# Kernel optimization log

Hardware: AMD Instinct MI355X
Metric: run time of the kernel (lower is better)

Reference implementation:

```python
import jax, jax.numpy as jnp
import numpy as np

B = 4_194_304  # batch
M = 4          # num_modes
N = 4          # num_nodes (hardcoded in BistableModeBank)
MU_MIN, MU_MAX = 0.1, 1.5


def setup_inputs() -> dict:
    key = jax.random.key(0)
    k1, k2, k3, k4, k5, k6 = jax.random.split(key, 6)
    return {
        "X": jax.random.normal(k1, (B, N), dtype=jnp.float32),
        "z": jax.random.randint(k2, (B,), 0, M, dtype=jnp.int32),
        "dt_val": jnp.full((1,), 0.01, dtype=jnp.float32),
        # learned params (torch inits them to zeros; small noise for non-degenerate test)
        "graph_logits": 0.1 * jax.random.normal(k3, (M, N, N), dtype=jnp.float32),
        "mu_logits": 0.1 * jax.random.normal(k4, (M, N), dtype=jnp.float32),
        "alpha_param": 0.1 * jax.random.normal(k5, (M,), dtype=jnp.float32),
        "beta_param": 0.1 * jax.random.normal(k6, (M,), dtype=jnp.float32),
    }


def reference(X, z, dt_val, graph_logits, mu_logits, alpha_param, beta_param):
    # graphs(): symmetrize logits, sigmoid, zero diagonal
    S = 0.5 * (graph_logits + jnp.swapaxes(graph_logits, 1, 2))
    W = jax.nn.sigmoid(S) * (1.0 - jnp.eye(N, dtype=X.dtype))  # (M,N,N)
    mus = MU_MIN + (MU_MAX - MU_MIN) * jax.nn.sigmoid(mu_logits)  # (M,N)
    deg = W.sum(axis=-1)  # (M,N)

    # per-item mode routing (replaces boolean-mask gather/scatter of forward_grouped)
    mu_z = mus[z]                        # (B,N)
    deg_z = deg[z]                       # (B,N)
    a_z = alpha_param[z][:, None]        # (B,1)
    b_z = beta_param[z][:, None]         # (B,1)

    local = mu_z * X - X ** 3            # bistable_batch
    # adjacency matmul for all modes, then select routed mode per item
    coup_all = jnp.einsum('mij,bj->bmi', W, X)                       # (B,M,N)
    coup_z = jnp.take_along_axis(coup_all, z[:, None, None], axis=1)[:, 0, :]  # (B,N)

    coupling = a_z * deg_z * X + b_z * coup_z
    dt = dt_val[0]
    return X + dt * (local + coupling)
```

## Files before the change

### kernel.cpp

```cpp
#include <hip/hip_runtime.h>


typedef float fvec4 __attribute__((ext_vector_type(4)));

__global__ __launch_bounds__(256) void bistable_kernel(
    const float* __restrict__ X,
    const int*   __restrict__ z,
    const float* __restrict__ dt_val,
    const float* __restrict__ G,
    const float* __restrict__ mu_logits,
    const float* __restrict__ alpha_p,
    const float* __restrict__ beta_p,
    float* __restrict__ out,
    int Bn)
{
    __shared__ float A[4 * 16];
    __shared__ float s_dt;

    const int t = threadIdx.x;
    if (t < 16) {
        const int m = t >> 2;
        const int i = t & 3;
        const float dt = dt_val[0];
        float w[4];
        float deg = 0.0f;
        #pragma unroll
        for (int j = 0; j < 4; ++j) {
            float s = 0.5f * (G[m * 16 + i * 4 + j] + G[m * 16 + j * 4 + i]);
            float wv = 1.0f / (1.0f + __expf(-s));
            if (j == i) wv = 0.0f;
            w[j] = wv;
            deg += wv;
        }
        const float mu = 0.1f + 1.4f / (1.0f + __expf(-mu_logits[m * 4 + i]));
        const float a = alpha_p[m];
        const float b = beta_p[m];
        float arow[4];
        #pragma unroll
        for (int j = 0; j < 4; ++j) arow[j] = dt * b * w[j];
        arow[i] = 1.0f + dt * (mu + a * deg);
        #pragma unroll
        for (int j = 0; j < 4; ++j) A[m * 16 + i * 4 + j] = arow[j];
    }
    if (t == 0) s_dt = dt_val[0];
    __syncthreads();

    const float dt = s_dt;
    const fvec4* __restrict__ X4 = (const fvec4*)X;
    fvec4* __restrict__ O4 = (fvec4*)out;

    const int tid = blockIdx.x * blockDim.x + t;
    const int stride = gridDim.x * blockDim.x;

    auto body = [&](const fvec4& xv, int m, fvec4& ov) {
        const float* __restrict__ a = &A[m * 16];
        const float x0 = xv.x, x1 = xv.y, x2 = xv.z, x3 = xv.w;
        ov.x = a[0]  * x0 + a[1]  * x1 + a[2]  * x2 + a[3]  * x3 - dt * x0 * x0 * x0;
        ov.y = a[4]  * x0 + a[5]  * x1 + a[6]  * x2 + a[7]  * x3 - dt * x1 * x1 * x1;
        ov.z = a[8]  * x0 + a[9]  * x1 + a[10] * x2 + a[11] * x3 - dt * x2 * x2 * x2;
        ov.w = a[12] * x0 + a[13] * x1 + a[14] * x2 + a[15] * x3 - dt * x3 * x3 * x3;
    };

    int idx = tid;
    for (; idx + 3 * stride < Bn; idx += 4 * stride) {
        const int i0 = idx, i1 = idx + stride, i2 = idx + 2 * stride, i3 = idx + 3 * stride;
        const fvec4 x0 = X4[i0];
        const fvec4 x1 = X4[i1];
        const fvec4 x2 = X4[i2];
        const fvec4 x3 = X4[i3];
        const int m0 = z[i0], m1 = z[i1], m2 = z[i2], m3 = z[i3];
        fvec4 o0, o1, o2, o3;
        body(x0, m0, o0);
        body(x1, m1, o1);
        body(x2, m2, o2);
        body(x3, m3, o3);
        __builtin_nontemporal_store(o0, &O4[i0]);
        __builtin_nontemporal_store(o1, &O4[i1]);
        __builtin_nontemporal_store(o2, &O4[i2]);
        __builtin_nontemporal_store(o3, &O4[i3]);
    }
    for (; idx < Bn; idx += stride) {
        const fvec4 xv = X4[idx];
        const int m = z[idx];
        fvec4 ov;
        body(xv, m, ov);
        __builtin_nontemporal_store(ov, &O4[idx]);
    }
}

extern "C" void kernel_launch(void* const* d_in, const int* in_sizes, int n_in,
                              void* d_out, int out_size, void* d_ws, size_t ws_size,
                              hipStream_t stream) {
    const float* X         = (const float*)d_in[0];
    const int*   z         = (const int*)d_in[1];
    const float* dt_val    = (const float*)d_in[2];
    const float* G         = (const float*)d_in[3];
    const float* mu_logits = (const float*)d_in[4];
    const float* alpha_p   = (const float*)d_in[5];
    const float* beta_p    = (const float*)d_in[6];
    float* out = (float*)d_out;

    const int Bn = in_sizes[1];

    const int block = 256;
    int grid = (Bn + block - 1) / block;
    if (grid > 4096) grid = 4096;

    bistable_kernel<<<grid, block, 0, stream>>>(X, z, dt_val, G, mu_logits,
                                                alpha_p, beta_p, out, Bn);
}
```

Before: 29.36 us.

## Software-pipeline grid-stride loop with two-deep register prefetch and halve grid cap

Replaces the 4-way unrolled grid-stride loop with a software-pipelined loop. Each thread keeps the current item and the next one in registers and issues the load for the item two strides ahead before computing and storing the current one. The grid cap drops from 4096 to 2048 blocks, so each thread handles more iterations. The aim is to keep loads in flight continuously, but there are fewer independent loads per thread than with the 4-way unroll, and the smaller grid may reduce memory-level parallelism on a bandwidth-bound kernel.

Measured after the change: 28.24 us. -3.8%, faster.

```diff
diff --git a/kernel.cpp b/kernel.cpp
--- a/kernel.cpp
+++ b/kernel.cpp
@@ -61,30 +61,32 @@
         ov.w = a[12] * x0 + a[13] * x1 + a[14] * x2 + a[15] * x3 - dt * x3 * x3 * x3;
     };
 
+    if (tid >= Bn) return;
+
+    fvec4 xa, xb, xn;
+    int   ma, mb, mn;
+
     int idx = tid;
-    for (; idx + 3 * stride < Bn; idx += 4 * stride) {
-        const int i0 = idx, i1 = idx + stride, i2 = idx + 2 * stride, i3 = idx + 3 * stride;
-        const fvec4 x0 = X4[i0];
-        const fvec4 x1 = X4[i1];
-        const fvec4 x2 = X4[i2];
-        const fvec4 x3 = X4[i3];
-        const int m0 = z[i0], m1 = z[i1], m2 = z[i2], m3 = z[i3];
-        fvec4 o0, o1, o2, o3;
-        body(x0, m0, o0);
-        body(x1, m1, o1);
-        body(x2, m2, o2);
-        body(x3, m3, o3);
-        __builtin_nontemporal_store(o0, &O4[i0]);
-        __builtin_nontemporal_store(o1, &O4[i1]);
-        __builtin_nontemporal_store(o2, &O4[i2]);
-        __builtin_nontemporal_store(o3, &O4[i3]);
+    xa = X4[idx]; ma = z[idx];
+    {
+        const int i1 = idx + stride;
+        if (i1 < Bn) { xb = X4[i1]; mb = z[i1]; }
+        else         { xb = xa;     mb = 0;     }
     }
-    for (; idx < Bn; idx += stride) {
-        const fvec4 xv = X4[idx];
-        const int m = z[idx];
+
+    for (;;) {
+        const int i2 = idx + 2 * stride;
+        const bool have2 = (i2 < Bn);
+        if (have2) { xn = X4[i2]; mn = z[i2]; }
+
         fvec4 ov;
-        body(xv, m, ov);
+        body(xa, ma, ov);
         __builtin_nontemporal_store(ov, &O4[idx]);
+
+        idx += stride;
+        if (idx >= Bn) break;
+        xa = xb; ma = mb;
+        if (have2) { xb = xn; mb = mn; }
     }
 }
 
@@ -104,7 +106,7 @@
 
     const int block = 256;
     int grid = (Bn + block - 1) / block;
-    if (grid > 4096) grid = 4096;
+    if (grid > 2048) grid = 2048;
 
     bistable_kernel<<<grid, block, 0, stream>>>(X, z, dt_val, G, mu_logits,
                                                 alpha_p, beta_p, out, Bn);
```
